# Kernel optimization log

Hardware: AMD Instinct MI355X
Metric: run time of the kernel (lower is better)

Reference implementation:

```python
import jax, jax.numpy as jnp
import numpy as np

CHUNK = 128  # scan_chunk_tokens


def _phi(x, w1, b1, w2, b2):
    # Linear -> SiLU -> Linear, applied over last dim
    h = x @ w1 + b1
    h = h * jax.nn.sigmoid(h)  # SiLU
    return h @ w2 + b2


def _chunked_scan(qp, kp, vv):
    # qp,kp: (BH, N, F); vv: (BH, N, D). Causal linear-attention chunked scan.
    BH, N, F = qp.shape
    D = vv.shape[-1]
    nC = N // CHUNK
    qc = qp.reshape(BH, nC, CHUNK, F).transpose(1, 0, 2, 3)  # (nC, BH, C, F)
    kc = kp.reshape(BH, nC, CHUNK, F).transpose(1, 0, 2, 3)
    vc = vv.reshape(BH, nC, CHUNK, D).transpose(1, 0, 2, 3)  # (nC, BH, C, D)

    def step(w_state, xs):
        qch, kch, vch = xs  # (BH, C, F), (BH, C, F), (BH, C, D)
        kv = jnp.einsum('bnf,bnv->bnfv', kch, vch)          # outer products
        w_prefix = jnp.cumsum(kv, axis=1) + w_state[:, None]  # inclusive prefix state
        out = jnp.einsum('bnf,bnfv->bnv', qch, w_prefix)
        return w_prefix[:, -1], out

    w0 = jnp.zeros((BH, F, D), dtype=qp.dtype)
    _, outs = jax.lax.scan(step, w0, (qc, kc, vc))  # outs: (nC, BH, C, D)
    return outs.transpose(1, 0, 2, 3).reshape(BH, N, D)


def setup_inputs() -> dict:
    key = jax.random.key(0)
    ks = jax.random.split(key, 7)
    B, H, N, D, F = 1, 24, 4096, 128, 256
    q = jax.random.normal(ks[0], (B, H, N, D), dtype=jnp.float32)
    k = jax.random.normal(ks[1], (B, H, N, D), dtype=jnp.float32)
    v = jax.random.normal(ks[2], (B, H, N, D), dtype=jnp.float32)
    # phi_net params: Linear(D->F), Linear(F->F)
    w1 = jax.random.normal(ks[3], (D, F), dtype=jnp.float32) / np.sqrt(D)
    b1 = jnp.zeros((F,), dtype=jnp.float32)
    w2 = jax.random.normal(ks[4], (F, F), dtype=jnp.float32) / np.sqrt(F)
    b2 = jnp.zeros((F,), dtype=jnp.float32)
    return {"q": q, "k": k, "v": v, "w1": w1, "b1": b1, "w2": w2, "b2": b2}


def reference(q, k, v, w1, b1, w2, b2):
    B, H, N, D = q.shape
    qf = q.reshape(B * H, N, D)
    kf = k.reshape(B * H, N, D)
    vf = v.reshape(B * H, N, D)
    q_phi = _phi(qf, w1, b1, w2, b2)
    k_phi = _phi(kf, w1, b1, w2, b2)
    inv_counts = jnp.arange(1, N + 1, dtype=q.dtype)[None, :, None]  # (1, N, 1)
    out_fwd = _chunked_scan(q_phi, k_phi, vf) / inv_counts
    out_rev = _chunked_scan(
        jnp.flip(q_phi, axis=1), jnp.flip(k_phi, axis=1), jnp.flip(vf, axis=1)
    ) / inv_counts
    out = out_fwd + jnp.flip(out_rev, axis=1)
    return out.reshape(B, H, N, D)
```

## Files before the change

### kernel.cpp

```cpp
#include <hip/hip_runtime.h>

#define BH  24
#define SEQ 4096
#define DIM 128
#define FF  256
#define CHK 128
#define NC  32
#define SLOT (FF*DIM)

typedef unsigned short u16;
typedef unsigned int   u32;
typedef short  s16x8 __attribute__((ext_vector_type(8)));
typedef float  f32x4 __attribute__((ext_vector_type(4)));

#define MFMA16(a,b,c) __builtin_amdgcn_mfma_f32_16x16x32_bf16(a,b,c,0,0,0)

static __device__ __forceinline__ float bf2f(u16 u) {
    return __uint_as_float(((u32)u) << 16);
}
static __device__ __forceinline__ u16 f2bf(float f) {
    u32 u = __float_as_uint(f);
    u += 0x7fffu + ((u >> 16) & 1u);
    return (u16)(u >> 16);
}

__global__ __launch_bounds__(256) void prep_kernel(
    const float* __restrict__ w1, const float* __restrict__ w2,
    u16* __restrict__ w1t, u16* __restrict__ w2t)
{
    int idx = blockIdx.x * 256 + threadIdx.x;
    int stride = gridDim.x * 256;
    for (int i = idx; i < 256*136; i += stride) {
        int f = i / 136, d = i - f*136;
        w1t[i] = (d < 128) ? f2bf(w1[d*FF + f]) : (u16)0;
    }
    for (int i = idx; i < 256*264; i += stride) {
        int e = i / 264, f = i - e*264;
        w2t[i] = (f < 256) ? f2bf(w2[f*FF + e]) : (u16)0;
    }
}

#define PTOK 64
#define XS_OFF   0
#define HS_OFF   0
#define YB_OFF   0
#define ARENA_U16 16896

__global__ __launch_bounds__(512) void phi_fused_kernel(
    const float* __restrict__ xq, const float* __restrict__ xk,
    const float* __restrict__ b1, const float* __restrict__ b2,
    const u16* __restrict__ w1t, const u16* __restrict__ w2t,
    u16* __restrict__ yq, u16* __restrict__ yk)
{
    __shared__ __align__(16) u16 arena[ARENA_U16];
    const int tid = threadIdx.x;
    int b = blockIdx.x;
    const int nB = (BH*SEQ)/PTOK;
    const float* xin; u16* yout;
    if (b < nB) { xin = xq; yout = yq; }
    else        { xin = xk; yout = yk; b -= nB; }
    const size_t tok0 = (size_t)b * PTOK;

    const int w = tid >> 6, lane = tid & 63;
    const int m = lane & 15, q = lane >> 4;
    const int wr = w >> 2, wc = w & 3;
    const f32x4 zero4 = {0.f, 0.f, 0.f, 0.f};

    {
        const float4* xsrc = reinterpret_cast<const float4*>(xin + tok0*DIM);
        for (int i = tid; i < PTOK*DIM/4; i += 512) {
            int row = i >> 5, c4 = i & 31;
            float4 xv = xsrc[i];
            u32 lo = (u32)f2bf(xv.x) | ((u32)f2bf(xv.y) << 16);
            u32 hi = (u32)f2bf(xv.z) | ((u32)f2bf(xv.w) << 16);
            *reinterpret_cast<uint2*>(arena + XS_OFF + row*136 + c4*4) = make_uint2(lo, hi);
        }
    }
    __syncthreads();

    f32x4 acc[2][4];
    #pragma unroll
    for (int i = 0; i < 2; ++i)
        #pragma unroll
        for (int ct = 0; ct < 4; ++ct) acc[i][ct] = zero4;

    #pragma unroll
    for (int kk = 0; kk < 4; ++kk) {
        int ko = kk*32 + q*8;
        s16x8 a[2], bb[4];
        #pragma unroll
        for (int ct = 0; ct < 4; ++ct)
            bb[ct] = *reinterpret_cast<const s16x8*>(w1t + (size_t)(wc*64 + ct*16 + m)*136 + ko);
        #pragma unroll
        for (int i = 0; i < 2; ++i)
            a[i] = *reinterpret_cast<const s16x8*>(arena + XS_OFF + (wr*32 + i*16 + m)*136 + ko);
        #pragma unroll
        for (int i = 0; i < 2; ++i)
            #pragma unroll
            for (int ct = 0; ct < 4; ++ct)
                acc[i][ct] = MFMA16(a[i], bb[ct], acc[i][ct]);
    }
    __syncthreads();

    {
        float b1v[4];
        #pragma unroll
        for (int ct = 0; ct < 4; ++ct) b1v[ct] = b1[wc*64 + ct*16 + m];
        #pragma unroll
        for (int i = 0; i < 2; ++i) {
            #pragma unroll
            for (int ct = 0; ct < 4; ++ct) {
                #pragma unroll
                for (int reg = 0; reg < 4; ++reg) {
                    float h = acc[i][ct][reg] + b1v[ct];
                    h = h / (1.0f + __expf(-h));
                    arena[HS_OFF + (size_t)(wr*32 + i*16 + q*4 + reg)*264 + (wc*64 + ct*16 + m)] = f2bf(h);
                }
            }
        }
    }
    __syncthreads();

    f32x4 acc2[2][4];
    #pragma unroll
    for (int i = 0; i < 2; ++i)
        #pragma unroll
        for (int ct = 0; ct < 4; ++ct) acc2[i][ct] = zero4;

    #pragma unroll
    for (int kk = 0; kk < 8; ++kk) {
        int ko = kk*32 + q*8;
        s16x8 a[2], bb[4];
        #pragma unroll
        for (int ct = 0; ct < 4; ++ct)
            bb[ct] = *reinterpret_cast<const s16x8*>(w2t + (size_t)(wc*64 + ct*16 + m)*264 + ko);
        #pragma unroll
        for (int i = 0; i < 2; ++i)
            a[i] = *reinterpret_cast<const s16x8*>(arena + HS_OFF + (wr*32 + i*16 + m)*264 + ko);
        #pragma unroll
        for (int i = 0; i < 2; ++i)
            #pragma unroll
            for (int ct = 0; ct < 4; ++ct)
                acc2[i][ct] = MFMA16(a[i], bb[ct], acc2[i][ct]);
    }
    __syncthreads();

    {
        float b2v[4];
        #pragma unroll
        for (int ct = 0; ct < 4; ++ct) b2v[ct] = b2[wc*64 + ct*16 + m];
        #pragma unroll
        for (int i = 0; i < 2; ++i) {
            #pragma unroll
            for (int ct = 0; ct < 4; ++ct) {
                #pragma unroll
                for (int reg = 0; reg < 4; ++reg) {
                    float y = acc2[i][ct][reg] + b2v[ct];
                    arena[YB_OFF + (size_t)(wr*32 + i*16 + q*4 + reg)*264 + (wc*64 + ct*16 + m)] = f2bf(y);
                }
            }
        }
    }
    __syncthreads();
    {
        uint4* dst = reinterpret_cast<uint4*>(yout + tok0*FF);
        const uint4* srcy = reinterpret_cast<const uint4*>(arena + YB_OFF);
        for (int i = tid; i < PTOK*32; i += 512) {
            int row = i >> 5, c = i & 31;
            dst[i] = srcy[row*33 + c];
        }
    }
}

#define KVA_OFF 0
#define KVB_OFF (128*72)
#define KV_U16  (128*72 + 256*72)

__global__ __launch_bounds__(256) void kvsum_kernel(
    const u16* __restrict__ kphi, const float* __restrict__ v,
    u16* __restrict__ chunkT)
{
    __shared__ __align__(16) u16 kv[KV_U16];
    const int c = blockIdx.x, h = blockIdx.y, tid = threadIdx.x;
    const int w = tid >> 6, lane = tid & 63;
    const int m = lane & 15, q = lane >> 4;
    const int wr = w >> 1, wc = w & 1;
    const size_t tok0 = (size_t)h*SEQ + (size_t)c*CHK;
    const f32x4 zero4 = {0.f, 0.f, 0.f, 0.f};

    f32x4 acc[8][4];
    #pragma unroll
    for (int i = 0; i < 8; ++i)
        #pragma unroll
        for (int ct = 0; ct < 4; ++ct) acc[i][ct] = zero4;

    for (int tc = 0; tc < 2; ++tc) {
        {
            const u16* kb = kphi + (tok0 + tc*64)*FF + tid;
            #pragma unroll
            for (int tg = 0; tg < 8; ++tg) {
                u16 vals[8];
                #pragma unroll
                for (int tt = 0; tt < 8; ++tt)
                    vals[tt] = kb[(size_t)(tg*8 + tt)*FF];
                uint4 p;
                p.x = (u32)vals[0] | ((u32)vals[1] << 16);
                p.y = (u32)vals[2] | ((u32)vals[3] << 16);
                p.z = (u32)vals[4] | ((u32)vals[5] << 16);
                p.w = (u32)vals[6] | ((u32)vals[7] << 16);
                *reinterpret_cast<uint4*>(kv + KVB_OFF + tid*72 + tg*8) = p;
            }
        }
        {
            const int d  = tid & 127;
            const int th = tid >> 7;
            const float* vb = v + (tok0 + tc*64 + th*32)*DIM + d;
            #pragma unroll
            for (int tg = 0; tg < 4; ++tg) {
                float fv[8];
                #pragma unroll
                for (int tt = 0; tt < 8; ++tt)
                    fv[tt] = vb[(size_t)(tg*8 + tt)*DIM];
                uint4 p;
                p.x = (u32)f2bf(fv[0]) | ((u32)f2bf(fv[1]) << 16);
                p.y = (u32)f2bf(fv[2]) | ((u32)f2bf(fv[3]) << 16);
                p.z = (u32)f2bf(fv[4]) | ((u32)f2bf(fv[5]) << 16);
                p.w = (u32)f2bf(fv[6]) | ((u32)f2bf(fv[7]) << 16);
                *reinterpret_cast<uint4*>(kv + KVA_OFF + d*72 + th*32 + tg*8) = p;
            }
        }
        __syncthreads();

        #pragma unroll
        for (int k2 = 0; k2 < 2; ++k2) {
            const int ko = k2*32 + q*8;
            s16x8 a[8], bb[4];
            #pragma unroll
            for (int i = 0; i < 8; ++i)
                a[i] = *reinterpret_cast<const s16x8*>(kv + KVB_OFF + (wc*128 + i*16 + m)*72 + ko);
            #pragma unroll
            for (int ct = 0; ct < 4; ++ct)
                bb[ct] = *reinterpret_cast<const s16x8*>(kv + KVA_OFF + (wr*64 + ct*16 + m)*72 + ko);
            #pragma unroll
            for (int i = 0; i < 8; ++i)
                #pragma unroll
                for (int ct = 0; ct < 4; ++ct)
                    acc[i][ct] = MFMA16(a[i], bb[ct], acc[i][ct]);
        }
        __syncthreads();
    }

    u16* outp = chunkT + (size_t)(h*NC + c)*SLOT;
    #pragma unroll
    for (int i = 0; i < 8; ++i) {
        const int f0 = wc*128 + i*16 + q*4;
        #pragma unroll
        for (int ct = 0; ct < 4; ++ct) {
            const int d = wr*64 + ct*16 + m;
            u32 lo = (u32)f2bf(acc[i][ct][0]) | ((u32)f2bf(acc[i][ct][1]) << 16);
            u32 hi = (u32)f2bf(acc[i][ct][2]) | ((u32)f2bf(acc[i][ct][3]) << 16);
            *reinterpret_cast<uint2*>(outp + (size_t)d*FF + f0) = make_uint2(lo, hi);
        }
    }
}

__global__ __launch_bounds__(256) void scan_kernel(
    u16* __restrict__ chunkT, u16* __restrict__ sufT)
{
    const int g = blockIdx.x * 256 + threadIdx.x;
    const int h = g >> 12;
    const int e = (g & 4095) * 8;
    u16* base  = chunkT + (size_t)h*NC*SLOT + e;
    u16* sbase = sufT   + (size_t)h*NC*SLOT + e;

    float tot[8];
    #pragma unroll
    for (int i = 0; i < 8; ++i) tot[i] = 0.f;
    for (int c = 0; c < NC; ++c) {
        uint4 r = *reinterpret_cast<const uint4*>(base + (size_t)c*SLOT);
        tot[0] += __uint_as_float(r.x << 16);
        tot[1] += __uint_as_float(r.x & 0xffff0000u);
        tot[2] += __uint_as_float(r.y << 16);
        tot[3] += __uint_as_float(r.y & 0xffff0000u);
        tot[4] += __uint_as_float(r.z << 16);
        tot[5] += __uint_as_float(r.z & 0xffff0000u);
        tot[6] += __uint_as_float(r.w << 16);
        tot[7] += __uint_as_float(r.w & 0xffff0000u);
    }
    float run[8];
    #pragma unroll
    for (int i = 0; i < 8; ++i) run[i] = 0.f;
    for (int c = 0; c < NC; ++c) {
        uint4 r = *reinterpret_cast<const uint4*>(base + (size_t)c*SLOT);
        float old[8];
        old[0] = __uint_as_float(r.x << 16);
        old[1] = __uint_as_float(r.x & 0xffff0000u);
        old[2] = __uint_as_float(r.y << 16);
        old[3] = __uint_as_float(r.y & 0xffff0000u);
        old[4] = __uint_as_float(r.z << 16);
        old[5] = __uint_as_float(r.z & 0xffff0000u);
        old[6] = __uint_as_float(r.w << 16);
        old[7] = __uint_as_float(r.w & 0xffff0000u);
        uint4 wp, wsuf;
        wp.x = (u32)f2bf(run[0]) | ((u32)f2bf(run[1]) << 16);
        wp.y = (u32)f2bf(run[2]) | ((u32)f2bf(run[3]) << 16);
        wp.z = (u32)f2bf(run[4]) | ((u32)f2bf(run[5]) << 16);
        wp.w = (u32)f2bf(run[6]) | ((u32)f2bf(run[7]) << 16);
        *reinterpret_cast<uint4*>(base + (size_t)c*SLOT) = wp;
        #pragma unroll
        for (int i = 0; i < 8; ++i) run[i] += old[i];
        float sf[8];
        #pragma unroll
        for (int i = 0; i < 8; ++i) sf[i] = tot[i] - run[i];
        wsuf.x = (u32)f2bf(sf[0]) | ((u32)f2bf(sf[1]) << 16);
        wsuf.y = (u32)f2bf(sf[2]) | ((u32)f2bf(sf[3]) << 16);
        wsuf.z = (u32)f2bf(sf[4]) | ((u32)f2bf(sf[5]) << 16);
        wsuf.w = (u32)f2bf(sf[6]) | ((u32)f2bf(sf[7]) << 16);
        *reinterpret_cast<uint4*>(sbase + (size_t)c*SLOT) = wsuf;
    }
}

#define VT_OFF 0
#define SF_OFF (128*136)
#define WB_OFF (2*128*136)
#define OARENA_U16 (2*128*136 + 128*264)

__global__ __launch_bounds__(512, 2) void out_kernel(
    const u16* __restrict__ qphi, const u16* __restrict__ kphi,
    const float* __restrict__ v,
    const u16* __restrict__ prefT, const u16* __restrict__ sufT,
    float* __restrict__ out)
{
    __shared__ __align__(16) u16 arena[OARENA_U16];
    const int c = blockIdx.x, h = blockIdx.y;
    const int tid = threadIdx.x;
    const int w = tid >> 6, lane = tid & 63;
    const int m = lane & 15, q = lane >> 4;
    const size_t tok0 = (size_t)h*SEQ + (size_t)c*CHK;
    const u16* qbase = qphi + tok0*FF;
    const int R = w*16;
    const int rowA = R + m;
    const f32x4 zero4 = {0.f, 0.f, 0.f, 0.f};

    {
        const int d  = tid & 127;
        const int j0 = (tid >> 7) * 8;
        const float* vb = v + tok0*DIM + d;
        #pragma unroll
        for (int jb = 0; jb < 4; ++jb) {
            const int jbase = jb*32 + j0;
            float vals[8];
            #pragma unroll
            for (int t = 0; t < 8; ++t) vals[t] = vb[(size_t)(jbase + t)*DIM];
            uint4 p;
            p.x = (u32)f2bf(vals[0]) | ((u32)f2bf(vals[1]) << 16);
            p.y = (u32)f2bf(vals[2]) | ((u32)f2bf(vals[3]) << 16);
            p.z = (u32)f2bf(vals[4]) | ((u32)f2bf(vals[5]) << 16);
            p.w = (u32)f2bf(vals[6]) | ((u32)f2bf(vals[7]) << 16);
            *reinterpret_cast<uint4*>(arena + VT_OFF + d*136 + jbase) = p;
        }
    }
    {
        const uint4* src = reinterpret_cast<const uint4*>(kphi + tok0*FF);
        uint4* dst = reinterpret_cast<uint4*>(arena + WB_OFF);
        for (int i = tid; i < 128*32; i += 512) {
            int row = i >> 5, cc = i & 31;
            dst[row*33 + cc] = src[i];
        }
    }
    __syncthreads();

    s16x8 qreg[8];
    #pragma unroll
    for (int kk = 0; kk < 8; ++kk)
        qreg[kk] = *reinterpret_cast<const s16x8*>(qbase + (size_t)rowA*FF + kk*32 + q*8);

    {
        f32x4 sacc[8];
        #pragma unroll
        for (int ct = 0; ct < 8; ++ct) sacc[ct] = zero4;
        for (int kk = 0; kk < 8; ++kk) {
            const int ko = kk*32 + q*8;
            #pragma unroll
            for (int ct = 0; ct < 8; ++ct) {
                s16x8 b = *reinterpret_cast<const s16x8*>(arena + WB_OFF + (size_t)(ct*16 + m)*264 + ko);
                sacc[ct] = MFMA16(qreg[kk], b, sacc[ct]);
            }
        }
        #pragma unroll
        for (int ct = 0; ct < 8; ++ct) {
            #pragma unroll
            for (int reg = 0; reg < 4; ++reg)
                arena[SF_OFF + (size_t)(R + q*4 + reg)*136 + (ct*16 + m)] = f2bf(sacc[ct][reg]);
        }
    }
    __syncthreads();

    f32x4 accA[8], accB[8];
    #pragma unroll
    for (int ct = 0; ct < 8; ++ct) { accA[ct] = zero4; accB[ct] = zero4; }

    uint4 stg[8];
    {
        const uint4* src = reinterpret_cast<const uint4*>(prefT + (size_t)(h*NC + c)*SLOT);
        #pragma unroll
        for (int i = 0; i < 8; ++i) stg[i] = src[tid + i*512];
    }

    #pragma unroll
    for (int kk = 0; kk < 4; ++kk) {
        const int ko = kk*32 + q*8;
        s16x8 b[8];
        #pragma unroll
        for (int ct = 0; ct < 8; ++ct)
            b[ct] = *reinterpret_cast<const s16x8*>(arena + VT_OFF + (size_t)(ct*16 + m)*136 + ko);
        const bool anyLow  = (kk*32       <= R + 15);
        const bool lowFull = (kk*32 + 31  <= R);
        const bool anyUp   = (kk*32 + 31  >= R);
        const bool upFull  = (kk*32       >= R + 16);
        s16x8 a = *reinterpret_cast<const s16x8*>(arena + SF_OFF + (size_t)rowA*136 + ko);
        if (anyLow) {
            s16x8 aL;
            if (lowFull) aL = a;
            else {
                #pragma unroll
                for (int e = 0; e < 8; ++e)
                    aL[e] = (kk*32 + q*8 + e <= rowA) ? a[e] : (short)0;
            }
            #pragma unroll
            for (int ct = 0; ct < 8; ++ct)
                accA[ct] = MFMA16(aL, b[ct], accA[ct]);
        }
        if (anyUp) {
            s16x8 aU;
            if (upFull) aU = a;
            else {
                #pragma unroll
                for (int e = 0; e < 8; ++e)
                    aU[e] = (kk*32 + q*8 + e >= rowA) ? a[e] : (short)0;
            }
            #pragma unroll
            for (int ct = 0; ct < 8; ++ct)
                accB[ct] = MFMA16(aU, b[ct], accB[ct]);
        }
    }

    {
        uint4* dst = reinterpret_cast<uint4*>(arena + WB_OFF);
        #pragma unroll
        for (int i = 0; i < 8; ++i) {
            int idx = tid + i*512;
            int row = idx >> 5, cc = idx & 31;
            dst[row*33 + cc] = stg[i];
        }
    }
    __syncthreads();

    {
        const uint4* src = reinterpret_cast<const uint4*>(sufT + (size_t)(h*NC + c)*SLOT);
        #pragma unroll
        for (int i = 0; i < 8; ++i) stg[i] = src[tid + i*512];
    }

    for (int kk = 0; kk < 8; ++kk) {
        const int ko = kk*32 + q*8;
        #pragma unroll
        for (int nt = 0; nt < 8; ++nt) {
            s16x8 bp = *reinterpret_cast<const s16x8*>(arena + WB_OFF + (size_t)(nt*16 + m)*264 + ko);
            accA[nt] = MFMA16(qreg[kk], bp, accA[nt]);
        }
    }

    {
        uint4* dst = reinterpret_cast<uint4*>(arena);
        #pragma unroll
        for (int i = 0; i < 8; ++i) {
            int idx = tid + i*512;
            int row = idx >> 5, cc = idx & 31;
            dst[row*33 + cc] = stg[i];
        }
    }
    __syncthreads();

    for (int kk = 0; kk < 8; ++kk) {
        const int ko = kk*32 + q*8;
        #pragma unroll
        for (int nt = 0; nt < 8; ++nt) {
            s16x8 bs = *reinterpret_cast<const s16x8*>(arena + (size_t)(nt*16 + m)*264 + ko);
            accB[nt] = MFMA16(qreg[kk], bs, accB[nt]);
        }
    }

    #pragma unroll
    for (int reg = 0; reg < 4; ++reg) {
        const int row = R + q*4 + reg;
        const int pos = c*CHK + row;
        const float ia = 1.0f / (float)(pos + 1);
        const float ib = 1.0f / (float)(SEQ - pos);
        float* orow = out + (tok0 + (size_t)row)*DIM;
        #pragma unroll
        for (int ct = 0; ct < 8; ++ct)
            orow[ct*16 + m] = accA[ct][reg]*ia + accB[ct][reg]*ib;
    }
}

extern "C" void kernel_launch(void* const* d_in, const int* in_sizes, int n_in,
                              void* d_out, int out_size, void* d_ws, size_t ws_size,
                              hipStream_t stream) {
    const float* q  = (const float*)d_in[0];
    const float* k  = (const float*)d_in[1];
    const float* v  = (const float*)d_in[2];
    const float* w1 = (const float*)d_in[3];
    const float* b1 = (const float*)d_in[4];
    const float* w2 = (const float*)d_in[5];
    const float* b2 = (const float*)d_in[6];
    float* out = (float*)d_out;

    char* ws = (char*)d_ws;
    const size_t phiBytes = (size_t)BH*SEQ*FF*sizeof(u16);
    u16* qphi   = (u16*)ws;
    u16* kphi   = (u16*)(ws + phiBytes);
    u16* chunkT = (u16*)(ws + 2*phiBytes);
    u16* sufT   = (u16*)(ws + 3*phiBytes);
    u16* w1t    = (u16*)(ws + 4*phiBytes);
    u16* w2t    = w1t + 256*136;

    prep_kernel<<<dim3(100), 256, 0, stream>>>(w1, w2, w1t, w2t);
    phi_fused_kernel<<<dim3(2*(BH*SEQ)/PTOK), 512, 0, stream>>>(q, k, b1, b2, w1t, w2t, qphi, kphi);
    kvsum_kernel<<<dim3(NC, BH), 256, 0, stream>>>(kphi, v, chunkT);
    scan_kernel<<<dim3(384), 256, 0, stream>>>(chunkT, sufT);
    out_kernel<<<dim3(NC, BH), 512, 0, stream>>>(qphi, kphi, v, chunkT, sufT, out);
}
```

Before: 390.1 us.

## Transpose phi GEMM operand roles and use packed bf16 conversion instructions

The phi kernel swaps MFMA operands so weights feed the A side and tokens the B side. Each lane then holds four consecutive feature outputs per token, so bias loads become float4 and results are written as packed uint2 stores straight to global memory. This drops the LDS staging of the second GEMM output and one barrier. Every kernel also replaces the manual round-to-nearest float-to-bf16 packing with the hardware v_cvt_pk_bf16_f32 instruction, which cuts ALU work but relies on the hardware rounding behaviour matching the manual version.

```diff
diff --git a/kernel.cpp b/kernel.cpp
--- a/kernel.cpp
+++ b/kernel.cpp
@@ -22,6 +22,11 @@
     u32 u = __float_as_uint(f);
     u += 0x7fffu + ((u >> 16) & 1u);
     return (u16)(u >> 16);
+}
+static __device__ __forceinline__ u32 cvtpk(float lo, float hi) {
+    u32 r;
+    asm("v_cvt_pk_bf16_f32 %0, %1, %2" : "=v"(r) : "v"(lo), "v"(hi));
+    return r;
 }
 
 __global__ __launch_bounds__(256) void prep_kernel(
@@ -43,7 +48,6 @@
 #define PTOK 64
 #define XS_OFF   0
 #define HS_OFF   0
-#define YB_OFF   0
 #define ARENA_U16 16896
 
 __global__ __launch_bounds__(512) void phi_fused_kernel(
@@ -63,7 +67,7 @@
 
     const int w = tid >> 6, lane = tid & 63;
     const int m = lane & 15, q = lane >> 4;
-    const int wr = w >> 2, wc = w & 3;
+    const int wf = w & 3, wt = w >> 2;
     const f32x4 zero4 = {0.f, 0.f, 0.f, 0.f};
 
     {
@@ -71,103 +75,92 @@
         for (int i = tid; i < PTOK*DIM/4; i += 512) {
             int row = i >> 5, c4 = i & 31;
             float4 xv = xsrc[i];
-            u32 lo = (u32)f2bf(xv.x) | ((u32)f2bf(xv.y) << 16);
-            u32 hi = (u32)f2bf(xv.z) | ((u32)f2bf(xv.w) << 16);
-            *reinterpret_cast<uint2*>(arena + XS_OFF + row*136 + c4*4) = make_uint2(lo, hi);
-        }
-    }
-    __syncthreads();
-
-    f32x4 acc[2][4];
-    #pragma unroll
-    for (int i = 0; i < 2; ++i)
-        #pragma unroll
-        for (int ct = 0; ct < 4; ++ct) acc[i][ct] = zero4;
+            *reinterpret_cast<uint2*>(arena + XS_OFF + row*136 + c4*4) =
+                make_uint2(cvtpk(xv.x, xv.y), cvtpk(xv.z, xv.w));
+        }
+    }
+    __syncthreads();
+
+    f32x4 acc[4][2];
+    #pragma unroll
+    for (int fi = 0; fi < 4; ++fi)
+        #pragma unroll
+        for (int tj = 0; tj < 2; ++tj) acc[fi][tj] = zero4;
 
     #pragma unroll
     for (int kk = 0; kk < 4; ++kk) {
-        int ko = kk*32 + q*8;
-        s16x8 a[2], bb[4];
-        #pragma unroll
-        for (int ct = 0; ct < 4; ++ct)
-            bb[ct] = *reinterpret_cast<const s16x8*>(w1t + (size_t)(wc*64 + ct*16 + m)*136 + ko);
-        #pragma unroll
-        for (int i = 0; i < 2; ++i)
-            a[i] = *reinterpret_cast<const s16x8*>(arena + XS_OFF + (wr*32 + i*16 + m)*136 + ko);
-        #pragma unroll
-        for (int i = 0; i < 2; ++i)
-            #pragma unroll
-            for (int ct = 0; ct < 4; ++ct)
-                acc[i][ct] = MFMA16(a[i], bb[ct], acc[i][ct]);
-    }
-    __syncthreads();
-
-    {
-        float b1v[4];
-        #pragma unroll
-        for (int ct = 0; ct < 4; ++ct) b1v[ct] = b1[wc*64 + ct*16 + m];
-        #pragma unroll
-        for (int i = 0; i < 2; ++i) {
-            #pragma unroll
-            for (int ct = 0; ct < 4; ++ct) {
-                #pragma unroll
-                for (int reg = 0; reg < 4; ++reg) {
-                    float h = acc[i][ct][reg] + b1v[ct];
-                    h = h / (1.0f + __expf(-h));
-                    arena[HS_OFF + (size_t)(wr*32 + i*16 + q*4 + reg)*264 + (wc*64 + ct*16 + m)] = f2bf(h);
-                }
-            }
-        }
-    }
-    __syncthreads();
-
-    f32x4 acc2[2][4];
-    #pragma unroll
-    for (int i = 0; i < 2; ++i)
-        #pragma unroll
-        for (int ct = 0; ct < 4; ++ct) acc2[i][ct] = zero4;
+        const int ko = kk*32 + q*8;
+        s16x8 a[4], bb[2];
+        #pragma unroll
+        for (int fi = 0; fi < 4; ++fi)
+            a[fi] = *reinterpret_cast<const s16x8*>(w1t + (size_t)(wf*64 + fi*16 + m)*136 + ko);
+        #pragma unroll
+        for (int tj = 0; tj < 2; ++tj)
+            bb[tj] = *reinterpret_cast<const s16x8*>(arena + XS_OFF + (wt*32 + tj*16 + m)*136 + ko);
+        #pragma unroll
+        for (int fi = 0; fi < 4; ++fi)
+            #pragma unroll
+            for (int tj = 0; tj < 2; ++tj)
+                acc[fi][tj] = MFMA16(a[fi], bb[tj], acc[fi][tj]);
+    }
+    __syncthreads();
+
+    #pragma unroll
+    for (int fi = 0; fi < 4; ++fi) {
+        const int f0 = wf*64 + fi*16 + q*4;
+        const float4 b1v = *reinterpret_cast<const float4*>(b1 + f0);
+        #pragma unroll
+        for (int tj = 0; tj < 2; ++tj) {
+            const int token = wt*32 + tj*16 + m;
+            float h[4];
+            h[0] = acc[fi][tj][0] + b1v.x;
+            h[1] = acc[fi][tj][1] + b1v.y;
+            h[2] = acc[fi][tj][2] + b1v.z;
+            h[3] = acc[fi][tj][3] + b1v.w;
+            #pragma unroll
+            for (int r = 0; r < 4; ++r) h[r] = h[r] / (1.0f + __expf(-h[r]));
+            *reinterpret_cast<uint2*>(arena + HS_OFF + (size_t)token*264 + f0) =
+                make_uint2(cvtpk(h[0], h[1]), cvtpk(h[2], h[3]));
+        }
+    }
+    __syncthreads();
+
+    f32x4 acc2[4][2];
+    #pragma unroll
+    for (int ei = 0; ei < 4; ++ei)
+        #pragma unroll
+        for (int tj = 0; tj < 2; ++tj) acc2[ei][tj] = zero4;
 
     #pragma unroll
     for (int kk = 0; kk < 8; ++kk) {
-        int ko = kk*32 + q*8;
-        s16x8 a[2], bb[4];
-        #pragma unroll
-        for (int ct = 0; ct < 4; ++ct)
-            bb[ct] = *reinterpret_cast<const s16x8*>(w2t + (size_t)(wc*64 + ct*16 + m)*264 + ko);
-        #pragma unroll
-        for (int i = 0; i < 2; ++i)
-            a[i] = *reinterpret_cast<const s16x8*>(arena + HS_OFF + (wr*32 + i*16 + m)*264 + ko);
-        #pragma unroll
-        for (int i = 0; i < 2; ++i)
-            #pragma unroll
-            for (int ct = 0; ct < 4; ++ct)
-                acc2[i][ct] = MFMA16(a[i], bb[ct], acc2[i][ct]);
-    }
-    __syncthreads();
-
-    {
-        float b2v[4];
-        #pragma unroll
-        for (int ct = 0; ct < 4; ++ct) b2v[ct] = b2[wc*64 + ct*16 + m];
-        #pragma unroll
-        for (int i = 0; i < 2; ++i) {
-            #pragma unroll
-            for (int ct = 0; ct < 4; ++ct) {
-                #pragma unroll
-                for (int reg = 0; reg < 4; ++reg) {
-                    float y = acc2[i][ct][reg] + b2v[ct];
-                    arena[YB_OFF + (size_t)(wr*32 + i*16 + q*4 + reg)*264 + (wc*64 + ct*16 + m)] = f2bf(y);
-                }
-            }
-        }
-    }
-    __syncthreads();
-    {
-        uint4* dst = reinterpret_cast<uint4*>(yout + tok0*FF);
-        const uint4* srcy = reinterpret_cast<const uint4*>(arena + YB_OFF);
-        for (int i = tid; i < PTOK*32; i += 512) {
-            int row = i >> 5, c = i & 31;
-            dst[i] = srcy[row*33 + c];
+        const int ko = kk*32 + q*8;
+        s16x8 a[4], bb[2];
+        #pragma unroll
+        for (int ei = 0; ei < 4; ++ei)
+            a[ei] = *reinterpret_cast<const s16x8*>(w2t + (size_t)(wf*64 + ei*16 + m)*264 + ko);
+        #pragma unroll
+        for (int tj = 0; tj < 2; ++tj)
+            bb[tj] = *reinterpret_cast<const s16x8*>(arena + HS_OFF + (size_t)(wt*32 + tj*16 + m)*264 + ko);
+        #pragma unroll
+        for (int ei = 0; ei < 4; ++ei)
+            #pragma unroll
+            for (int tj = 0; tj < 2; ++tj)
+                acc2[ei][tj] = MFMA16(a[ei], bb[tj], acc2[ei][tj]);
+    }
+
+    #pragma unroll
+    for (int ei = 0; ei < 4; ++ei) {
+        const int e0 = wf*64 + ei*16 + q*4;
+        const float4 b2v = *reinterpret_cast<const float4*>(b2 + e0);
+        #pragma unroll
+        for (int tj = 0; tj < 2; ++tj) {
+            const int token = wt*32 + tj*16 + m;
+            float y0 = acc2[ei][tj][0] + b2v.x;
+            float y1 = acc2[ei][tj][1] + b2v.y;
+            float y2 = acc2[ei][tj][2] + b2v.z;
+            float y3 = acc2[ei][tj][3] + b2v.w;
+            *reinterpret_cast<uint2*>(yout + (tok0 + token)*FF + e0) =
+                make_uint2(cvtpk(y0, y1), cvtpk(y2, y3));
         }
     }
 }
@@ -222,10 +215,10 @@
                 for (int tt = 0; tt < 8; ++tt)
                     fv[tt] = vb[(size_t)(tg*8 + tt)*DIM];
                 uint4 p;
-                p.x = (u32)f2bf(fv[0]) | ((u32)f2bf(fv[1]) << 16);
-                p.y = (u32)f2bf(fv[2]) | ((u32)f2bf(fv[3]) << 16);
-                p.z = (u32)f2bf(fv[4]) | ((u32)f2bf(fv[5]) << 16);
-                p.w = (u32)f2bf(fv[6]) | ((u32)f2bf(fv[7]) << 16);
+                p.x = cvtpk(fv[0], fv[1]);
+                p.y = cvtpk(fv[2], fv[3]);
+                p.z = cvtpk(fv[4], fv[5]);
+                p.w = cvtpk(fv[6], fv[7]);
                 *reinterpret_cast<uint4*>(kv + KVA_OFF + d*72 + th*32 + tg*8) = p;
             }
         }
@@ -257,9 +250,9 @@
         #pragma unroll
         for (int ct = 0; ct < 4; ++ct) {
             const int d = wr*64 + ct*16 + m;
-            u32 lo = (u32)f2bf(acc[i][ct][0]) | ((u32)f2bf(acc[i][ct][1]) << 16);
-            u32 hi = (u32)f2bf(acc[i][ct][2]) | ((u32)f2bf(acc[i][ct][3]) << 16);
-            *reinterpret_cast<uint2*>(outp + (size_t)d*FF + f0) = make_uint2(lo, hi);
+            *reinterpret_cast<uint2*>(outp + (size_t)d*FF + f0) =
+                make_uint2(cvtpk(acc[i][ct][0], acc[i][ct][1]),
+                           cvtpk(acc[i][ct][2], acc[i][ct][3]));
         }
     }
 }
@@ -302,20 +295,20 @@
         old[6] = __uint_as_float(r.w << 16);
         old[7] = __uint_as_float(r.w & 0xffff0000u);
         uint4 wp, wsuf;
-        wp.x = (u32)f2bf(run[0]) | ((u32)f2bf(run[1]) << 16);
-        wp.y = (u32)f2bf(run[2]) | ((u32)f2bf(run[3]) << 16);
-        wp.z = (u32)f2bf(run[4]) | ((u32)f2bf(run[5]) << 16);
-        wp.w = (u32)f2bf(run[6]) | ((u32)f2bf(run[7]) << 16);
+        wp.x = cvtpk(run[0], run[1]);
+        wp.y = cvtpk(run[2], run[3]);
+        wp.z = cvtpk(run[4], run[5]);
+        wp.w = cvtpk(run[6], run[7]);
         *reinterpret_cast<uint4*>(base + (size_t)c*SLOT) = wp;
         #pragma unroll
         for (int i = 0; i < 8; ++i) run[i] += old[i];
         float sf[8];
         #pragma unroll
         for (int i = 0; i < 8; ++i) sf[i] = tot[i] - run[i];
-        wsuf.x = (u32)f2bf(sf[0]) | ((u32)f2bf(sf[1]) << 16);
-        wsuf.y = (u32)f2bf(sf[2]) | ((u32)f2bf(sf[3]) << 16);
-        wsuf.z = (u32)f2bf(sf[4]) | ((u32)f2bf(sf[5]) << 16);
-        wsuf.w = (u32)f2bf(sf[6]) | ((u32)f2bf(sf[7]) << 16);
+        wsuf.x = cvtpk(sf[0], sf[1]);
+        wsuf.y = cvtpk(sf[2], sf[3]);
+        wsuf.z = cvtpk(sf[4], sf[5]);
+        wsuf.w = cvtpk(sf[6], sf[7]);
         *reinterpret_cast<uint4*>(sbase + (size_t)c*SLOT) = wsuf;
     }
 }
@@ -353,10 +346,10 @@
             #pragma unroll
             for (int t = 0; t < 8; ++t) vals[t] = vb[(size_t)(jbase + t)*DIM];
             uint4 p;
-            p.x = (u32)f2bf(vals[0]) | ((u32)f2bf(vals[1]) << 16);
-            p.y = (u32)f2bf(vals[2]) | ((u32)f2bf(vals[3]) << 16);
-            p.z = (u32)f2bf(vals[4]) | ((u32)f2bf(vals[5]) << 16);
-            p.w = (u32)f2bf(vals[6]) | ((u32)f2bf(vals[7]) << 16);
+            p.x = cvtpk(vals[0], vals[1]);
+            p.y = cvtpk(vals[2], vals[3]);
+            p.z = cvtpk(vals[4], vals[5]);
+            p.w = cvtpk(vals[6], vals[7]);
             *reinterpret_cast<uint4*>(arena + VT_OFF + d*136 + jbase) = p;
         }
     }
```

Result: slower. 410.3 us (+5.2%).
